# Kernel tuning notes

Measured on AMD Instinct MI355X. Metric: run time of the kernel, lower is better.

## Reference

```python
import jax, jax.numpy as jnp
import numpy as np

B, S, D = 2, 2048, 1024
H, DK, DV = 16, 64, 64


def setup_inputs() -> dict:
    key = jax.random.key(0)
    ks = jax.random.split(key, 10)
    scale = 0.02
    return {
        "x": jax.random.normal(ks[0], (B, S, D), dtype=jnp.float32),
        "Wq": jax.random.normal(ks[1], (D, H * DK), dtype=jnp.float32) * scale,
        "bq": jax.random.normal(ks[2], (H * DK,), dtype=jnp.float32) * scale,
        "Wk": jax.random.normal(ks[3], (D, H * DK), dtype=jnp.float32) * scale,
        "bk": jax.random.normal(ks[4], (H * DK,), dtype=jnp.float32) * scale,
        "Wv": jax.random.normal(ks[5], (D, H * DV), dtype=jnp.float32) * scale,
        "bv": jax.random.normal(ks[6], (H * DV,), dtype=jnp.float32) * scale,
        "Wo": jax.random.normal(ks[7], (H * DV, D), dtype=jnp.float32) * scale,
        "bo": jax.random.normal(ks[8], (D,), dtype=jnp.float32) * scale,
    }


def reference(x, Wq, bq, Wk, bk, Wv, bv, Wo, bo):
    b, s, d = x.shape
    # projections -> (b, H, s, dk/dv)
    q = (x @ Wq + bq).reshape(b, s, H, DK).transpose(0, 2, 1, 3)
    k = (x @ Wk + bk).reshape(b, s, H, DK).transpose(0, 2, 1, 3)
    v = (x @ Wv + bv).reshape(b, s, H, DV).transpose(0, 2, 1, 3)
    # scaled QK^T: (b, H, s, s)
    scores = jnp.einsum("bhqd,bhkd->bhqk", q, k) / np.sqrt(DK).astype(np.float32)
    # sign-based reweighting: scores * sign(scores) (zeros -> sign 1) == |scores|
    reweighted = jnp.abs(scores)
    # causal mask: lower triangle keeps value, strict upper -> -inf (value * -inf)
    causal = jnp.tril(jnp.ones((s, s), dtype=bool))
    logits = jnp.where(causal, reweighted, -jnp.inf)
    w = jax.nn.softmax(logits, axis=-1)
    o = jnp.einsum("bhqk,bhkd->bhqd", w, v)  # (b, H, s, DV)
    o = o.transpose(0, 2, 1, 3).reshape(b, s, H * DV)
    return o @ Wo + bo
```

## Files before the change

### kernel.cpp

```cpp
#include <hip/hip_runtime.h>


#define DI __device__ __forceinline__

typedef __bf16 bf16x8 __attribute__((ext_vector_type(8)));
typedef float f32x4 __attribute__((ext_vector_type(4)));
typedef unsigned short u16x8 __attribute__((ext_vector_type(8)));
typedef unsigned short u16x4 __attribute__((ext_vector_type(4)));

union U8 { u16x8 u; bf16x8 b; };
union PB { unsigned int w[4]; u16x8 u; bf16x8 b; };

typedef const __attribute__((address_space(1))) unsigned int* gas_p;
typedef __attribute__((address_space(3))) unsigned int* las_p;

DI void gload16(const unsigned short* g, unsigned short* l) {
  __builtin_amdgcn_global_load_lds((gas_p)(const void*)g, (las_p)(void*)l, 16, 0, 0);
}

#define WAIT_VM4  asm volatile("s_waitcnt vmcnt(4)" ::: "memory")
#define WAIT_VM0  asm volatile("s_waitcnt vmcnt(0)" ::: "memory")
#define BARRIER   __builtin_amdgcn_s_barrier()

DI unsigned short f2bf(float f) {
  unsigned int u = __float_as_uint(f);
  u += 0x7FFFu + ((u >> 16) & 1u);
  return (unsigned short)(u >> 16);
}
DI float bf2f(unsigned short v) { return __uint_as_float((unsigned int)v << 16); }

__global__ void k_prep(
    const float* __restrict__ W0, const float* __restrict__ W1,
    const float* __restrict__ W2, const float* __restrict__ W3,
    unsigned short* __restrict__ T0, unsigned short* __restrict__ T1,
    unsigned short* __restrict__ T2, unsigned short* __restrict__ T3,
    const float* __restrict__ x, unsigned short* __restrict__ xb) {
  const int z = blockIdx.z;
  const int tx = threadIdx.x, ty = threadIdx.y;
  if (z >= 4) {
    int chunk = (z - 4) * 1024 + blockIdx.y * 32 + blockIdx.x;
    size_t i = ((size_t)chunk * 256 + ty * 32 + tx) * 4;
    float4 v = *(const float4*)(x + i);
    u16x4 o;
    o[0] = f2bf(v.x); o[1] = f2bf(v.y); o[2] = f2bf(v.z); o[3] = f2bf(v.w);
    *(u16x4*)(xb + i) = o;
    return;
  }
  const float* W = (z == 0) ? W0 : (z == 1) ? W1 : (z == 2) ? W2 : W3;
  unsigned short* T = (z == 0) ? T0 : (z == 1) ? T1 : (z == 2) ? T2 : T3;
  __shared__ unsigned short buf[32][33];
  const int k0 = blockIdx.x * 32, n0 = blockIdx.y * 32;
#pragma unroll
  for (int j = 0; j < 4; ++j) {
    int r = ty + j * 8;
    buf[r][tx] = f2bf(W[(size_t)(k0 + r) * 1024 + n0 + tx]);
  }
  __syncthreads();
#pragma unroll
  for (int j = 0; j < 4; ++j) {
    int c = ty + j * 8;
    T[(size_t)(n0 + c) * 1024 + k0 + tx] = buf[tx][c];
  }
}

DI void stage_gemm(const unsigned short* __restrict__ src, unsigned short* dst,
                   int row0, int k0, int tid, int wid) {
#pragma unroll
  for (int i = 0; i < 2; ++i) {
    int T = i * 256 + tid;
    int row = T >> 2, ch = T & 3;
    int sch = ch ^ (row & 3);
    gload16(&src[(size_t)(row0 + row) * 1024 + k0 + sch * 8],
            &dst[(i * 256 + wid * 64) * 8]);
  }
}

DI void gemm_main(const unsigned short* __restrict__ A,
                  const unsigned short* __restrict__ Bm,
                  unsigned short* As, unsigned short* Bs,
                  int m0, int n0, f32x4 acc[4][4]) {
  const int tid = threadIdx.x;
  const int lane = tid & 63, wid = tid >> 6;
  const int wr = wid >> 1, wc = wid & 1;
  const int g = lane >> 4, lq = lane & 15;

  stage_gemm(A, As, m0, 0, tid, wid);
  stage_gemm(Bm, Bs, n0, 0, tid, wid);
  __syncthreads();
  int buf = 0;
  for (int k0 = 0; k0 < 1024; k0 += 32) {
    if (k0 + 32 < 1024) {
      stage_gemm(A, As + (buf ^ 1) * 4096, m0, k0 + 32, tid, wid);
      stage_gemm(Bm, Bs + (buf ^ 1) * 4096, n0, k0 + 32, tid, wid);
    }
    const unsigned short* Ab = As + buf * 4096;
    const unsigned short* Bb = Bs + buf * 4096;
    U8 af[4], bfr[4];
#pragma unroll
    for (int f = 0; f < 4; ++f) {
      af[f].u  = *(const u16x8*)&Ab[(wr * 64 + f * 16 + lq) * 32 + ((g ^ (lq & 3)) * 8)];
      bfr[f].u = *(const u16x8*)&Bb[(wc * 64 + f * 16 + lq) * 32 + ((g ^ (lq & 3)) * 8)];
    }
#pragma unroll
    for (int i = 0; i < 4; ++i)
#pragma unroll
      for (int j = 0; j < 4; ++j)
        acc[i][j] = __builtin_amdgcn_mfma_f32_16x16x32_bf16(af[i].b, bfr[j].b,
                                                            acc[i][j], 0, 0, 0);
    __syncthreads();
    buf ^= 1;
  }
}

__global__ __launch_bounds__(256) void k_gemm_qkv(
    const unsigned short* __restrict__ xb,
    const unsigned short* __restrict__ Wqt, const unsigned short* __restrict__ Wkt,
    const unsigned short* __restrict__ Wvt,
    const float* __restrict__ bq, const float* __restrict__ bk,
    const float* __restrict__ bv,
    unsigned short* __restrict__ Qo, unsigned short* __restrict__ Ko,
    unsigned short* __restrict__ Vto) {
  __shared__ unsigned short Sh[128 * 136];
  unsigned short* As = Sh;
  unsigned short* Bs = Sh + 8192;
  const int z = blockIdx.z;
  const unsigned short* Bm = (z == 0) ? Wqt : (z == 1) ? Wkt : Wvt;
  const float* bias = (z == 0) ? bq : (z == 1) ? bk : bv;

  f32x4 acc[4][4];
#pragma unroll
  for (int i = 0; i < 4; ++i)
#pragma unroll
    for (int j = 0; j < 4; ++j) acc[i][j] = f32x4{0.f, 0.f, 0.f, 0.f};

  const int m0 = blockIdx.x * 128, n0 = blockIdx.y * 128;
  gemm_main(xb, Bm, As, Bs, m0, n0, acc);

  const int tid = threadIdx.x;
  const int lane = tid & 63, wid = tid >> 6;
  const int wr = wid >> 1, wc = wid & 1;
  const int g = lane >> 4, lq = lane & 15;
  const int bb = m0 >> 11;

#pragma unroll
  for (int j = 0; j < 4; ++j) {
    int col = wc * 64 + j * 16 + lq;
    float bv_ = bias[n0 + col];
#pragma unroll
    for (int i = 0; i < 4; ++i)
#pragma unroll
      for (int r = 0; r < 4; ++r) {
        int row = wr * 64 + i * 16 + g * 4 + r;
        Sh[row * 136 + col] = f2bf(acc[i][j][r] + bv_);
      }
  }
  __syncthreads();

  if (z < 2) {
    unsigned short* dstQK = (z == 0) ? Qo : Ko;
    const int ch = tid & 15, sb = tid >> 4;
#pragma unroll
    for (int it = 0; it < 8; ++it) {
      int s = sb + it * 16;
      u16x8 v = *(const u16x8*)&Sh[s * 136 + ch * 8];
      int gcol = n0 + ch * 8;
      int hh = gcol >> 6, dd = gcol & 63;
      int sr = (m0 + s) & 2047;
      *(u16x8*)&dstQK[(((size_t)(bb * 16 + hh)) * 2048 + sr) * 64 + dd] = v;
    }
  } else {
    const int d = tid & 127, hf = tid >> 7;
    int gcol = n0 + d;
    int hh = gcol >> 6, dd = gcol & 63;
    size_t vrow = ((size_t)(bb * 16 + hh)) * 64 + dd;
#pragma unroll
    for (int it = 0; it < 8; ++it) {
      int s0 = (hf + it * 2) * 8;
      u16x8 vv;
#pragma unroll
      for (int e = 0; e < 8; ++e) vv[e] = Sh[(s0 + e) * 136 + d];
      *(u16x8*)&Vto[vrow * 2048 + (m0 & 2047) + s0] = vv;
    }
  }
}

__global__ __launch_bounds__(256) void k_gemm_out(
    const unsigned short* __restrict__ Ob, const unsigned short* __restrict__ Wot,
    const float* __restrict__ bo, float* __restrict__ out) {
  __shared__ unsigned short As[2 * 4096];
  __shared__ unsigned short Bs[2 * 4096];
  f32x4 acc[4][4];
#pragma unroll
  for (int i = 0; i < 4; ++i)
#pragma unroll
    for (int j = 0; j < 4; ++j) acc[i][j] = f32x4{0.f, 0.f, 0.f, 0.f};

  const int m0 = blockIdx.x * 128, n0 = blockIdx.y * 128;
  gemm_main(Ob, Wot, As, Bs, m0, n0, acc);

  const int lane = threadIdx.x & 63, wid = threadIdx.x >> 6;
  const int wr = wid >> 1, wc = wid & 1;
  const int g = lane >> 4, lq = lane & 15;
#pragma unroll
  for (int j = 0; j < 4; ++j) {
    int col = n0 + wc * 64 + j * 16 + lq;
    float bv_ = bo[col];
#pragma unroll
    for (int i = 0; i < 4; ++i)
#pragma unroll
      for (int r = 0; r < 4; ++r) {
        int row = m0 + wr * 64 + i * 16 + g * 4 + r;
        out[(size_t)row * 1024 + col] = acc[i][j][r] + bv_;
      }
  }
}

template<bool MASKED>
DI void ptile(f32x4 sacc[4], f32x4& lacc, unsigned int pk[4][2],
              int qrow, int kk0, int g) {
  const float SC = 0.18033688011112042f;
#pragma unroll
  for (int c = 0; c < 4; ++c) {
#pragma unroll
    for (int r = 0; r < 4; ++r) {
      float sv = fabsf(sacc[c][r]) * SC;
      if (MASKED) {
        int k = kk0 + g * 8 + r + 4 * (c & 1) + 32 * (c >> 1);
        sv = (k <= qrow) ? sv : -1e30f;
      }
      float p = exp2f(sv);
      sacc[c][r] = p;
      lacc[r] += p;
    }
    asm("v_cvt_pk_bf16_f32 %0, %1, %2"
        : "=v"(pk[c][0]) : "v"(sacc[c][0]), "v"(sacc[c][1]));
    asm("v_cvt_pk_bf16_f32 %0, %1, %2"
        : "=v"(pk[c][1]) : "v"(sacc[c][2]), "v"(sacc[c][3]));
  }
}

DI void flash_dual(bool complete, int qblk, int t0, int t1, int slot,
                   const unsigned short* __restrict__ Q,
                   const unsigned short* __restrict__ Km,
                   const unsigned short* __restrict__ Vt,
                   unsigned short* __restrict__ O,
                   unsigned short* __restrict__ Pp, float* __restrict__ Lp,
                   unsigned short* Ks0, unsigned short* Vs0,
                   size_t qkbase, size_t vbase, int b, int h,
                   int tid, int wid, int g, int lq) {
  const int lrowA = wid * 32 + lq, lrowB = lrowA + 16;
  const int qrowA = qblk * 128 + lrowA, qrowB = qblk * 128 + lrowB;
  const int diag0 = 2 * qblk;

  auto stage = [&](int bf, int t) {
    const int kk0 = t * 64;
#pragma unroll
    for (int i = 0; i < 2; ++i) {
      int T = i * 256 + tid;
      int row = T >> 3, ch = T & 7;
      int sch = ch ^ (row & 7);
      gload16(&Km[qkbase + (size_t)(kk0 + row) * 64 + sch * 8],
              Ks0 + bf * 4096 + (i * 2048 + wid * 512));
      gload16(&Vt[vbase + (size_t)row * 2048 + kk0 + sch * 8],
              Vs0 + bf * 4096 + (i * 2048 + wid * 512));
    }
  };

  U8 aqA0, aqA1, aqB0, aqB1;
  {
    const unsigned short* qp = &Q[qkbase + (size_t)qrowA * 64 + g * 8];
    aqA0.u = *(const u16x8*)qp;
    aqA1.u = *(const u16x8*)(qp + 32);
    const unsigned short* qp2 = &Q[qkbase + (size_t)qrowB * 64 + g * 8];
    aqB0.u = *(const u16x8*)qp2;
    aqB1.u = *(const u16x8*)(qp2 + 32);
  }
  f32x4 laccA = f32x4{0.f, 0.f, 0.f, 0.f}, laccB = f32x4{0.f, 0.f, 0.f, 0.f};
  f32x4 oaccA[4], oaccB[4];
#pragma unroll
  for (int c = 0; c < 4; ++c) {
    oaccA[c] = f32x4{0.f, 0.f, 0.f, 0.f};
    oaccB[c] = f32x4{0.f, 0.f, 0.f, 0.f};
  }

  const int rbase = (lq >> 2) * 8 + (lq & 3);

  stage(0, t0);
  if (t0 + 1 < t1) stage(1, t0 + 1);
  int bi = 0;
  for (int t = t0; t < t1; ++t) {
    if (t + 1 < t1) WAIT_VM4; else WAIT_VM0;
    BARRIER;
    if (t + 2 < t1) {
      int nb = bi + 2; if (nb >= 3) nb -= 3;
      stage(nb, t + 2);
    }
    const unsigned short* Kb = Ks0 + bi * 4096;
    const unsigned short* Vb = Vs0 + bi * 4096;
    const int kk0 = t * 64;
    f32x4 saccA[4], saccB[4];
    __builtin_amdgcn_s_setprio(1);
#pragma unroll
    for (int c = 0; c < 4; ++c) {
      int row = rbase + 4 * (c & 1) + 32 * (c >> 1);
      int r7 = row & 7;
      U8 kf0, kf1;
      kf0.u = *(const u16x8*)&Kb[row * 64 + ((g ^ r7) * 8)];
      kf1.u = *(const u16x8*)&Kb[row * 64 + (((4 + g) ^ r7) * 8)];
      saccA[c] = __builtin_amdgcn_mfma_f32_16x16x32_bf16(kf0.b, aqA0.b,
                                                         f32x4{0.f, 0.f, 0.f, 0.f}, 0, 0, 0);
      saccA[c] = __builtin_amdgcn_mfma_f32_16x16x32_bf16(kf1.b, aqA1.b, saccA[c], 0, 0, 0);
      saccB[c] = __builtin_amdgcn_mfma_f32_16x16x32_bf16(kf0.b, aqB0.b,
                                                         f32x4{0.f, 0.f, 0.f, 0.f}, 0, 0, 0);
      saccB[c] = __builtin_amdgcn_mfma_f32_16x16x32_bf16(kf1.b, aqB1.b, saccB[c], 0, 0, 0);
    }
    __builtin_amdgcn_s_setprio(0);
    unsigned int pkA[4][2], pkB[4][2];
    if (t >= diag0) {
      ptile<true>(saccA, laccA, pkA, qrowA, kk0, g);
      ptile<true>(saccB, laccB, pkB, qrowB, kk0, g);
    } else {
      ptile<false>(saccA, laccA, pkA, qrowA, kk0, g);
      ptile<false>(saccB, laccB, pkB, qrowB, kk0, g);
    }
    __builtin_amdgcn_s_setprio(1);
#pragma unroll
    for (int hh = 0; hh < 2; ++hh) {
      PB pbA, pbB;
      pbA.w[0] = pkA[hh * 2 + 0][0]; pbA.w[1] = pkA[hh * 2 + 0][1];
      pbA.w[2] = pkA[hh * 2 + 1][0]; pbA.w[3] = pkA[hh * 2 + 1][1];
      pbB.w[0] = pkB[hh * 2 + 0][0]; pbB.w[1] = pkB[hh * 2 + 0][1];
      pbB.w[2] = pkB[hh * 2 + 1][0]; pbB.w[3] = pkB[hh * 2 + 1][1];
#pragma unroll
      for (int c = 0; c < 4; ++c) {
        U8 vf;
        vf.u = *(const u16x8*)&Vb[(c * 16 + lq) * 64 + (((hh * 4 + g) ^ (lq & 7)) * 8)];
        oaccA[c] = __builtin_amdgcn_mfma_f32_16x16x32_bf16(vf.b, pbA.b, oaccA[c], 0, 0, 0);
        oaccB[c] = __builtin_amdgcn_mfma_f32_16x16x32_bf16(vf.b, pbB.b, oaccB[c], 0, 0, 0);
      }
    }
    __builtin_amdgcn_s_setprio(0);
    ++bi; if (bi >= 3) bi = 0;
  }

  float lsA = (laccA[0] + laccA[1]) + (laccA[2] + laccA[3]);
  lsA += __shfl_xor(lsA, 16, 64);
  lsA += __shfl_xor(lsA, 32, 64);
  float lsB = (laccB[0] + laccB[1]) + (laccB[2] + laccB[3]);
  lsB += __shfl_xor(lsB, 16, 64);
  lsB += __shfl_xor(lsB, 32, 64);
  if (complete) {
    float invA = 1.0f / lsA, invB = 1.0f / lsB;
#pragma unroll
    for (int c = 0; c < 4; ++c) {
      u16x4 ovA, ovB;
#pragma unroll
      for (int r2 = 0; r2 < 4; ++r2) {
        ovA[r2] = f2bf(oaccA[c][r2] * invA);
        ovB[r2] = f2bf(oaccB[c][r2] * invB);
      }
      *(u16x4*)&O[((size_t)(b * 2048 + qrowA)) * 1024 + h * 64 + c * 16 + g * 4] = ovA;
      *(u16x4*)&O[((size_t)(b * 2048 + qrowB)) * 1024 + h * 64 + c * 16 + g * 4] = ovB;
    }
  } else {
    if (g == 0) {
      Lp[slot * 128 + lrowA] = lsA;
      Lp[slot * 128 + lrowB] = lsB;
    }
    size_t pbase = (size_t)slot * 8192;
#pragma unroll
    for (int c = 0; c < 4; ++c) {
      u16x4 ovA, ovB;
#pragma unroll
      for (int r2 = 0; r2 < 4; ++r2) {
        ovA[r2] = f2bf(oaccA[c][r2]);
        ovB[r2] = f2bf(oaccB[c][r2]);
      }
      *(u16x4*)&Pp[pbase + lrowA * 64 + c * 16 + g * 4] = ovA;
      *(u16x4*)&Pp[pbase + lrowB * 64 + c * 16 + g * 4] = ovB;
    }
  }
  WAIT_VM0;
  BARRIER;
}

__global__ __launch_bounds__(256) void k_flash(
    const unsigned short* __restrict__ Q, const unsigned short* __restrict__ Km,
    const unsigned short* __restrict__ Vt, unsigned short* __restrict__ O,
    unsigned short* __restrict__ Pp, float* __restrict__ Lp) {
  __shared__ unsigned short Ks[3 * 4096];
  __shared__ unsigned short Vs[3 * 4096];
  const int tid = threadIdx.x;
  const int lane = tid & 63, wid = tid >> 6;
  const int g = lane >> 4, lq = lane & 15;
  const int bid = blockIdx.x;
  const int xcd = bid & 7, idx = bid >> 3;
  const int bh = xcd * 4 + (idx >> 4);
  const int rr = idx & 15;
  const int p = rr >> 1, sp = rr & 1;
  const int mp = 15 - p;
  const int b = bh >> 4, h = bh & 15;
  const size_t qkbase = (size_t)bh * 2048 * 64;
  const size_t vbase = (size_t)bh * 64 * 2048;

  if (sp == 0) {
    flash_dual(true, p, 0, 2 * p + 2, 0, Q, Km, Vt, O, Pp, Lp,
               Ks, Vs, qkbase, vbase, b, h, tid, wid, g, lq);
    flash_dual(false, mp, 0, 15 - 2 * p, (bh * 8 + p) * 2 + 0, Q, Km, Vt, O, Pp, Lp,
               Ks, Vs, qkbase, vbase, b, h, tid, wid, g, lq);
  } else {
    flash_dual(false, mp, 15 - 2 * p, 32 - 2 * p, (bh * 8 + p) * 2 + 1, Q, Km, Vt, O, Pp, Lp,
               Ks, Vs, qkbase, vbase, b, h, tid, wid, g, lq);
  }
}

__global__ __launch_bounds__(256) void k_combine(
    const unsigned short* __restrict__ Pp, const float* __restrict__ Lp,
    unsigned short* __restrict__ O) {
  int gid = blockIdx.x * 256 + threadIdx.x;
  int dv4 = gid & 15;
  int q   = (gid >> 4) & 127;
  int pi  = (gid >> 11) & 7;
  int bh  = gid >> 14;
  int slot0 = (bh * 8 + pi) * 2;
  size_t base = (size_t)slot0 * 8192 + q * 64 + dv4 * 4;
  u16x4 a = *(const u16x4*)&Pp[base];
  u16x4 c = *(const u16x4*)&Pp[base + 8192];
  float l = Lp[slot0 * 128 + q] + Lp[(slot0 + 1) * 128 + q];
  float inv = 1.0f / l;
  u16x4 o;
#pragma unroll
  for (int r = 0; r < 4; ++r) o[r] = f2bf((bf2f(a[r]) + bf2f(c[r])) * inv);
  int b = bh >> 4, h = bh & 15;
  int srow = (15 - pi) * 128 + q;
  *(u16x4*)&O[((size_t)(b * 2048 + srow)) * 1024 + h * 64 + dv4 * 4] = o;
}

extern "C" void kernel_launch(void* const* d_in, const int* in_sizes, int n_in,
                              void* d_out, int out_size, void* d_ws, size_t ws_size,
                              hipStream_t stream) {
  const float* x  = (const float*)d_in[0];
  const float* Wq = (const float*)d_in[1];
  const float* bq = (const float*)d_in[2];
  const float* Wk = (const float*)d_in[3];
  const float* bk = (const float*)d_in[4];
  const float* Wv = (const float*)d_in[5];
  const float* bv = (const float*)d_in[6];
  const float* Wo = (const float*)d_in[7];
  const float* bo = (const float*)d_in[8];
  float* out = (float*)d_out;

  char* ws = (char*)d_ws;
  const size_t MB = 1024 * 1024;
  unsigned short* xb   = (unsigned short*)(ws + 0 * MB);
  unsigned short* Wqt  = (unsigned short*)(ws + 8 * MB);
  unsigned short* Wkt  = (unsigned short*)(ws + 10 * MB);
  unsigned short* Wvt  = (unsigned short*)(ws + 12 * MB);
  unsigned short* Wot  = (unsigned short*)(ws + 14 * MB);
  unsigned short* Qws  = (unsigned short*)(ws + 16 * MB);
  unsigned short* Kws  = (unsigned short*)(ws + 24 * MB);
  unsigned short* Vtws = (unsigned short*)(ws + 32 * MB);
  unsigned short* Ows  = (unsigned short*)(ws + 40 * MB);
  unsigned short* Pp   = (unsigned short*)(ws + 0 * MB);
  float*          Lp   = (float*)(ws + 8 * MB);

  k_prep<<<dim3(32, 32, 8), dim3(32, 8), 0, stream>>>(Wq, Wk, Wv, Wo,
                                                      Wqt, Wkt, Wvt, Wot, x, xb);
  k_gemm_qkv<<<dim3(32, 8, 3), 256, 0, stream>>>(xb, Wqt, Wkt, Wvt, bq, bk, bv,
                                                 Qws, Kws, Vtws);
  k_flash<<<512, 256, 0, stream>>>(Qws, Kws, Vtws, Ows, Pp, Lp);
  k_combine<<<2048, 256, 0, stream>>>(Pp, Lp, Ows);
  k_gemm_out<<<dim3(32, 8), 256, 0, stream>>>(Ows, Wot, bo, out);
}
```

Before: 109.2 us.

## Process paired query blocks together to share staged K/V tiles

In first-half workgroups, the diagonal query block and its mirrored partner now run in one loop over the same triple-buffered K/V tiles, instead of two sequential passes that each restage K/V from global memory. A per-p split point (T0) sets how many key tiles the partner block handles here versus in the second-half workgroup. The goal is to cut redundant global-to-LDS traffic and one pipeline warm-up and drain. In exchange, live accumulators and Q fragments double, which raises register pressure and may lower occupancy, and the new split leaves the two halves slightly uneven.

Measured after the change: 132.4 us. +21.2%, slower.

```diff
diff --git a/kernel.cpp b/kernel.cpp
--- a/kernel.cpp
+++ b/kernel.cpp
@@ -239,149 +239,102 @@
   }
 }
 
-DI void flash_dual(bool complete, int qblk, int t0, int t1, int slot,
-                   const unsigned short* __restrict__ Q,
-                   const unsigned short* __restrict__ Km,
-                   const unsigned short* __restrict__ Vt,
-                   unsigned short* __restrict__ O,
-                   unsigned short* __restrict__ Pp, float* __restrict__ Lp,
-                   unsigned short* Ks0, unsigned short* Vs0,
-                   size_t qkbase, size_t vbase, int b, int h,
-                   int tid, int wid, int g, int lq) {
-  const int lrowA = wid * 32 + lq, lrowB = lrowA + 16;
-  const int qrowA = qblk * 128 + lrowA, qrowB = qblk * 128 + lrowB;
-  const int diag0 = 2 * qblk;
-
-  auto stage = [&](int bf, int t) {
-    const int kk0 = t * 64;
-#pragma unroll
-    for (int i = 0; i < 2; ++i) {
-      int T = i * 256 + tid;
-      int row = T >> 3, ch = T & 7;
-      int sch = ch ^ (row & 7);
-      gload16(&Km[qkbase + (size_t)(kk0 + row) * 64 + sch * 8],
-              Ks0 + bf * 4096 + (i * 2048 + wid * 512));
-      gload16(&Vt[vbase + (size_t)row * 2048 + kk0 + sch * 8],
-              Vs0 + bf * 4096 + (i * 2048 + wid * 512));
-    }
-  };
-
-  U8 aqA0, aqA1, aqB0, aqB1;
-  {
-    const unsigned short* qp = &Q[qkbase + (size_t)qrowA * 64 + g * 8];
-    aqA0.u = *(const u16x8*)qp;
-    aqA1.u = *(const u16x8*)(qp + 32);
-    const unsigned short* qp2 = &Q[qkbase + (size_t)qrowB * 64 + g * 8];
-    aqB0.u = *(const u16x8*)qp2;
-    aqB1.u = *(const u16x8*)(qp2 + 32);
-  }
-  f32x4 laccA = f32x4{0.f, 0.f, 0.f, 0.f}, laccB = f32x4{0.f, 0.f, 0.f, 0.f};
-  f32x4 oaccA[4], oaccB[4];
+DI void qblock_step(bool masked, int qrowA, int qrowB, int kk0,
+                    const unsigned short* Kb, const unsigned short* Vb,
+                    const U8& aq0A, const U8& aq1A, const U8& aq0B, const U8& aq1B,
+                    f32x4& laccA, f32x4& laccB, f32x4 oaccA[4], f32x4 oaccB[4],
+                    int rbase, int g, int lq) {
+  f32x4 saccA[4], saccB[4];
+  __builtin_amdgcn_s_setprio(1);
 #pragma unroll
   for (int c = 0; c < 4; ++c) {
-    oaccA[c] = f32x4{0.f, 0.f, 0.f, 0.f};
-    oaccB[c] = f32x4{0.f, 0.f, 0.f, 0.f};
-  }
-
-  const int rbase = (lq >> 2) * 8 + (lq & 3);
-
-  stage(0, t0);
-  if (t0 + 1 < t1) stage(1, t0 + 1);
-  int bi = 0;
-  for (int t = t0; t < t1; ++t) {
-    if (t + 1 < t1) WAIT_VM4; else WAIT_VM0;
-    BARRIER;
-    if (t + 2 < t1) {
-      int nb = bi + 2; if (nb >= 3) nb -= 3;
-      stage(nb, t + 2);
-    }
-    const unsigned short* Kb = Ks0 + bi * 4096;
-    const unsigned short* Vb = Vs0 + bi * 4096;
-    const int kk0 = t * 64;
-    f32x4 saccA[4], saccB[4];
-    __builtin_amdgcn_s_setprio(1);
+    int row = rbase + 4 * (c & 1) + 32 * (c >> 1);
+    int r7 = row & 7;
+    U8 kf0, kf1;
+    kf0.u = *(const u16x8*)&Kb[row * 64 + ((g ^ r7) * 8)];
+    kf1.u = *(const u16x8*)&Kb[row * 64 + (((4 + g) ^ r7) * 8)];
+    saccA[c] = __builtin_amdgcn_mfma_f32_16x16x32_bf16(kf0.b, aq0A.b,
+                                                       f32x4{0.f, 0.f, 0.f, 0.f}, 0, 0, 0);
+    saccA[c] = __builtin_amdgcn_mfma_f32_16x16x32_bf16(kf1.b, aq1A.b, saccA[c], 0, 0, 0);
+    saccB[c] = __builtin_amdgcn_mfma_f32_16x16x32_bf16(kf0.b, aq0B.b,
+                                                       f32x4{0.f, 0.f, 0.f, 0.f}, 0, 0, 0);
+    saccB[c] = __builtin_amdgcn_mfma_f32_16x16x32_bf16(kf1.b, aq1B.b, saccB[c], 0, 0, 0);
+  }
+  __builtin_amdgcn_s_setprio(0);
+  unsigned int pkA[4][2], pkB[4][2];
+  if (masked) {
+    ptile<true>(saccA, laccA, pkA, qrowA, kk0, g);
+    ptile<true>(saccB, laccB, pkB, qrowB, kk0, g);
+  } else {
+    ptile<false>(saccA, laccA, pkA, qrowA, kk0, g);
+    ptile<false>(saccB, laccB, pkB, qrowB, kk0, g);
+  }
+  __builtin_amdgcn_s_setprio(1);
+#pragma unroll
+  for (int hh = 0; hh < 2; ++hh) {
+    PB pbA, pbB;
+    pbA.w[0] = pkA[hh * 2 + 0][0]; pbA.w[1] = pkA[hh * 2 + 0][1];
+    pbA.w[2] = pkA[hh * 2 + 1][0]; pbA.w[3] = pkA[hh * 2 + 1][1];
+    pbB.w[0] = pkB[hh * 2 + 0][0]; pbB.w[1] = pkB[hh * 2 + 0][1];
+    pbB.w[2] = pkB[hh * 2 + 1][0]; pbB.w[3] = pkB[hh * 2 + 1][1];
 #pragma unroll
     for (int c = 0; c < 4; ++c) {
-      int row = rbase + 4 * (c & 1) + 32 * (c >> 1);
-      int r7 = row & 7;
-      U8 kf0, kf1;
-      kf0.u = *(const u16x8*)&Kb[row * 64 + ((g ^ r7) * 8)];
-      kf1.u = *(const u16x8*)&Kb[row * 64 + (((4 + g) ^ r7) * 8)];
-      saccA[c] = __builtin_amdgcn_mfma_f32_16x16x32_bf16(kf0.b, aqA0.b,
-                                                         f32x4{0.f, 0.f, 0.f, 0.f}, 0, 0, 0);
-      saccA[c] = __builtin_amdgcn_mfma_f32_16x16x32_bf16(kf1.b, aqA1.b, saccA[c], 0, 0, 0);
-      saccB[c] = __builtin_amdgcn_mfma_f32_16x16x32_bf16(kf0.b, aqB0.b,
-                                                         f32x4{0.f, 0.f, 0.f, 0.f}, 0, 0, 0);
-      saccB[c] = __builtin_amdgcn_mfma_f32_16x16x32_bf16(kf1.b, aqB1.b, saccB[c], 0, 0, 0);
-    }
-    __builtin_amdgcn_s_setprio(0);
-    unsigned int pkA[4][2], pkB[4][2];
-    if (t >= diag0) {
-      ptile<true>(saccA, laccA, pkA, qrowA, kk0, g);
-      ptile<true>(saccB, laccB, pkB, qrowB, kk0, g);
-    } else {
-      ptile<false>(saccA, laccA, pkA, qrowA, kk0, g);
-      ptile<false>(saccB, laccB, pkB, qrowB, kk0, g);
-    }
-    __builtin_amdgcn_s_setprio(1);
-#pragma unroll
-    for (int hh = 0; hh < 2; ++hh) {
-      PB pbA, pbB;
-      pbA.w[0] = pkA[hh * 2 + 0][0]; pbA.w[1] = pkA[hh * 2 + 0][1];
-      pbA.w[2] = pkA[hh * 2 + 1][0]; pbA.w[3] = pkA[hh * 2 + 1][1];
-      pbB.w[0] = pkB[hh * 2 + 0][0]; pbB.w[1] = pkB[hh * 2 + 0][1];
-      pbB.w[2] = pkB[hh * 2 + 1][0]; pbB.w[3] = pkB[hh * 2 + 1][1];
-#pragma unroll
-      for (int c = 0; c < 4; ++c) {
-        U8 vf;
-        vf.u = *(const u16x8*)&Vb[(c * 16 + lq) * 64 + (((hh * 4 + g) ^ (lq & 7)) * 8)];
-        oaccA[c] = __builtin_amdgcn_mfma_f32_16x16x32_bf16(vf.b, pbA.b, oaccA[c], 0, 0, 0);
-        oaccB[c] = __builtin_amdgcn_mfma_f32_16x16x32_bf16(vf.b, pbB.b, oaccB[c], 0, 0, 0);
-      }
-    }
-    __builtin_amdgcn_s_setprio(0);
-    ++bi; if (bi >= 3) bi = 0;
-  }
-
+      U8 vf;
+      vf.u = *(const u16x8*)&Vb[(c * 16 + lq) * 64 + (((hh * 4 + g) ^ (lq & 7)) * 8)];
+      oaccA[c] = __builtin_amdgcn_mfma_f32_16x16x32_bf16(vf.b, pbA.b, oaccA[c], 0, 0, 0);
+      oaccB[c] = __builtin_amdgcn_mfma_f32_16x16x32_bf16(vf.b, pbB.b, oaccB[c], 0, 0, 0);
+    }
+  }
+  __builtin_amdgcn_s_setprio(0);
+}
+
+DI void epilogue_complete(f32x4 oaccA[4], f32x4 oaccB[4], f32x4& laccA, f32x4& laccB,
+                          unsigned short* O, int b, int h, int qrowA, int qrowB, int g) {
   float lsA = (laccA[0] + laccA[1]) + (laccA[2] + laccA[3]);
   lsA += __shfl_xor(lsA, 16, 64);
   lsA += __shfl_xor(lsA, 32, 64);
   float lsB = (laccB[0] + laccB[1]) + (laccB[2] + laccB[3]);
   lsB += __shfl_xor(lsB, 16, 64);
   lsB += __shfl_xor(lsB, 32, 64);
-  if (complete) {
-    float invA = 1.0f / lsA, invB = 1.0f / lsB;
-#pragma unroll
-    for (int c = 0; c < 4; ++c) {
-      u16x4 ovA, ovB;
-#pragma unroll
-      for (int r2 = 0; r2 < 4; ++r2) {
-        ovA[r2] = f2bf(oaccA[c][r2] * invA);
-        ovB[r2] = f2bf(oaccB[c][r2] * invB);
-      }
-      *(u16x4*)&O[((size_t)(b * 2048 + qrowA)) * 1024 + h * 64 + c * 16 + g * 4] = ovA;
-      *(u16x4*)&O[((size_t)(b * 2048 + qrowB)) * 1024 + h * 64 + c * 16 + g * 4] = ovB;
-    }
-  } else {
-    if (g == 0) {
-      Lp[slot * 128 + lrowA] = lsA;
-      Lp[slot * 128 + lrowB] = lsB;
-    }
-    size_t pbase = (size_t)slot * 8192;
-#pragma unroll
-    for (int c = 0; c < 4; ++c) {
-      u16x4 ovA, ovB;
-#pragma unroll
-      for (int r2 = 0; r2 < 4; ++r2) {
-        ovA[r2] = f2bf(oaccA[c][r2]);
-        ovB[r2] = f2bf(oaccB[c][r2]);
-      }
-      *(u16x4*)&Pp[pbase + lrowA * 64 + c * 16 + g * 4] = ovA;
-      *(u16x4*)&Pp[pbase + lrowB * 64 + c * 16 + g * 4] = ovB;
-    }
-  }
-  WAIT_VM0;
-  BARRIER;
+  float invA = 1.0f / lsA, invB = 1.0f / lsB;
+#pragma unroll
+  for (int c = 0; c < 4; ++c) {
+    u16x4 ovA, ovB;
+#pragma unroll
+    for (int r2 = 0; r2 < 4; ++r2) {
+      ovA[r2] = f2bf(oaccA[c][r2] * invA);
+      ovB[r2] = f2bf(oaccB[c][r2] * invB);
+    }
+    *(u16x4*)&O[((size_t)(b * 2048 + qrowA)) * 1024 + h * 64 + c * 16 + g * 4] = ovA;
+    *(u16x4*)&O[((size_t)(b * 2048 + qrowB)) * 1024 + h * 64 + c * 16 + g * 4] = ovB;
+  }
+}
+
+DI void epilogue_partial(f32x4 oaccA[4], f32x4 oaccB[4], f32x4& laccA, f32x4& laccB,
+                         unsigned short* Pp, float* Lp, int slot,
+                         int lrowA, int lrowB, int g) {
+  float lsA = (laccA[0] + laccA[1]) + (laccA[2] + laccA[3]);
+  lsA += __shfl_xor(lsA, 16, 64);
+  lsA += __shfl_xor(lsA, 32, 64);
+  float lsB = (laccB[0] + laccB[1]) + (laccB[2] + laccB[3]);
+  lsB += __shfl_xor(lsB, 16, 64);
+  lsB += __shfl_xor(lsB, 32, 64);
+  if (g == 0) {
+    Lp[slot * 128 + lrowA] = lsA;
+    Lp[slot * 128 + lrowB] = lsB;
+  }
+  size_t pbase = (size_t)slot * 8192;
+#pragma unroll
+  for (int c = 0; c < 4; ++c) {
+    u16x4 ovA, ovB;
+#pragma unroll
+    for (int r2 = 0; r2 < 4; ++r2) {
+      ovA[r2] = f2bf(oaccA[c][r2]);
+      ovB[r2] = f2bf(oaccB[c][r2]);
+    }
+    *(u16x4*)&Pp[pbase + lrowA * 64 + c * 16 + g * 4] = ovA;
+    *(u16x4*)&Pp[pbase + lrowB * 64 + c * 16 + g * 4] = ovB;
+  }
 }
 
 __global__ __launch_bounds__(256) void k_flash(
@@ -402,15 +355,118 @@
   const int b = bh >> 4, h = bh & 15;
   const size_t qkbase = (size_t)bh * 2048 * 64;
   const size_t vbase = (size_t)bh * 64 * 2048;
+  const int T0 = (p <= 4) ? (16 - p) : ((p == 5) ? 10 : ((p == 6) ? 6 : 2));
+  const int lrowA = wid * 32 + lq, lrowB = lrowA + 16;
+  const int rbase = (lq >> 2) * 8 + (lq & 3);
+
+  auto stage = [&](int bf, int t) {
+    const int kk0 = t * 64;
+#pragma unroll
+    for (int i = 0; i < 2; ++i) {
+      int T = i * 256 + tid;
+      int row = T >> 3, ch = T & 7;
+      int sch = ch ^ (row & 7);
+      gload16(&Km[qkbase + (size_t)(kk0 + row) * 64 + sch * 8],
+              Ks + bf * 4096 + (i * 2048 + wid * 512));
+      gload16(&Vt[vbase + (size_t)row * 2048 + kk0 + sch * 8],
+              Vs + bf * 4096 + (i * 2048 + wid * 512));
+    }
+  };
 
   if (sp == 0) {
-    flash_dual(true, p, 0, 2 * p + 2, 0, Q, Km, Vt, O, Pp, Lp,
-               Ks, Vs, qkbase, vbase, b, h, tid, wid, g, lq);
-    flash_dual(false, mp, 0, 15 - 2 * p, (bh * 8 + p) * 2 + 0, Q, Km, Vt, O, Pp, Lp,
-               Ks, Vs, qkbase, vbase, b, h, tid, wid, g, lq);
+    const int ntP = 2 * p + 2;
+    const int TE = (ntP > T0) ? ntP : T0;
+    const int qrowPA = p * 128 + lrowA, qrowPB = p * 128 + lrowB;
+    const int qrowMA = mp * 128 + lrowA, qrowMB = mp * 128 + lrowB;
+    const int diagP = 2 * p;
+
+    U8 aqPA0, aqPA1, aqPB0, aqPB1, aqMA0, aqMA1, aqMB0, aqMB1;
+    {
+      const unsigned short* qp;
+      qp = &Q[qkbase + (size_t)qrowPA * 64 + g * 8];
+      aqPA0.u = *(const u16x8*)qp; aqPA1.u = *(const u16x8*)(qp + 32);
+      qp = &Q[qkbase + (size_t)qrowPB * 64 + g * 8];
+      aqPB0.u = *(const u16x8*)qp; aqPB1.u = *(const u16x8*)(qp + 32);
+      qp = &Q[qkbase + (size_t)qrowMA * 64 + g * 8];
+      aqMA0.u = *(const u16x8*)qp; aqMA1.u = *(const u16x8*)(qp + 32);
+      qp = &Q[qkbase + (size_t)qrowMB * 64 + g * 8];
+      aqMB0.u = *(const u16x8*)qp; aqMB1.u = *(const u16x8*)(qp + 32);
+    }
+    f32x4 laccPA = f32x4{0.f,0.f,0.f,0.f}, laccPB = f32x4{0.f,0.f,0.f,0.f};
+    f32x4 laccMA = f32x4{0.f,0.f,0.f,0.f}, laccMB = f32x4{0.f,0.f,0.f,0.f};
+    f32x4 oaccPA[4], oaccPB[4], oaccMA[4], oaccMB[4];
+#pragma unroll
+    for (int c = 0; c < 4; ++c) {
+      oaccPA[c] = f32x4{0.f,0.f,0.f,0.f}; oaccPB[c] = f32x4{0.f,0.f,0.f,0.f};
+      oaccMA[c] = f32x4{0.f,0.f,0.f,0.f}; oaccMB[c] = f32x4{0.f,0.f,0.f,0.f};
+    }
+
+    stage(0, 0);
+    if (1 < TE) stage(1, 1);
+    int bi = 0;
+    for (int t = 0; t < TE; ++t) {
+      if (t + 1 < TE) WAIT_VM4; else WAIT_VM0;
+      BARRIER;
+      if (t + 2 < TE) {
+        int nb = bi + 2; if (nb >= 3) nb -= 3;
+        stage(nb, t + 2);
+      }
+      const unsigned short* Kb = Ks + bi * 4096;
+      const unsigned short* Vb = Vs + bi * 4096;
+      const int kk0 = t * 64;
+      if (t < ntP)
+        qblock_step(t >= diagP, qrowPA, qrowPB, kk0, Kb, Vb,
+                    aqPA0, aqPA1, aqPB0, aqPB1, laccPA, laccPB, oaccPA, oaccPB,
+                    rbase, g, lq);
+      if (t < T0)
+        qblock_step(false, qrowMA, qrowMB, kk0, Kb, Vb,
+                    aqMA0, aqMA1, aqMB0, aqMB1, laccMA, laccMB, oaccMA, oaccMB,
+                    rbase, g, lq);
+      ++bi; if (bi >= 3) bi = 0;
+    }
+    epilogue_complete(oaccPA, oaccPB, laccPA, laccPB, O, b, h, qrowPA, qrowPB, g);
+    epilogue_partial(oaccMA, oaccMB, laccMA, laccMB, Pp, Lp,
+                     (bh * 8 + p) * 2 + 0, lrowA, lrowB, g);
   } else {
-    flash_dual(false, mp, 15 - 2 * p, 32 - 2 * p, (bh * 8 + p) * 2 + 1, Q, Km, Vt, O, Pp, Lp,
-               Ks, Vs, qkbase, vbase, b, h, tid, wid, g, lq);
+    const int t0 = T0, t1 = 32 - 2 * p;
+    const int qrowMA = mp * 128 + lrowA, qrowMB = mp * 128 + lrowB;
+    const int diagM = 2 * mp;
+
+    U8 aqMA0, aqMA1, aqMB0, aqMB1;
+    {
+      const unsigned short* qp;
+      qp = &Q[qkbase + (size_t)qrowMA * 64 + g * 8];
+      aqMA0.u = *(const u16x8*)qp; aqMA1.u = *(const u16x8*)(qp + 32);
+      qp = &Q[qkbase + (size_t)qrowMB * 64 + g * 8];
+      aqMB0.u = *(const u16x8*)qp; aqMB1.u = *(const u16x8*)(qp + 32);
+    }
+    f32x4 laccMA = f32x4{0.f,0.f,0.f,0.f}, laccMB = f32x4{0.f,0.f,0.f,0.f};
+    f32x4 oaccMA[4], oaccMB[4];
+#pragma unroll
+    for (int c = 0; c < 4; ++c) {
+      oaccMA[c] = f32x4{0.f,0.f,0.f,0.f};
+      oaccMB[c] = f32x4{0.f,0.f,0.f,0.f};
+    }
+
+    stage(0, t0);
+    if (t0 + 1 < t1) stage(1, t0 + 1);
+    int bi = 0;
+    for (int t = t0; t < t1; ++t) {
+      if (t + 1 < t1) WAIT_VM4; else WAIT_VM0;
+      BARRIER;
+      if (t + 2 < t1) {
+        int nb = bi + 2; if (nb >= 3) nb -= 3;
+        stage(nb, t + 2);
+      }
+      const unsigned short* Kb = Ks + bi * 4096;
+      const unsigned short* Vb = Vs + bi * 4096;
+      qblock_step(t >= diagM, qrowMA, qrowMB, t * 64, Kb, Vb,
+                  aqMA0, aqMA1, aqMB0, aqMB1, laccMA, laccMB, oaccMA, oaccMB,
+                  rbase, g, lq);
+      ++bi; if (bi >= 3) bi = 0;
+    }
+    epilogue_partial(oaccMA, oaccMB, laccMA, laccMB, Pp, Lp,
+                     (bh * 8 + p) * 2 + 1, lrowA, lrowB, g);
   }
 }
 
```
